# Kernel tuning notes

Measured on AMD Instinct MI355X. Metric: run time of the kernel, lower is better.

Reference implementation:

```python
import jax, jax.numpy as jnp
import numpy as np

N = 50000        # total nodes (random mix of disease type=1 and mirna type=0)
E = 1250000      # edges, avg degree 25
D_SIM = 256      # similarity feature dim (G.ndata['d_sim']/['m_sim'] width)
F_ATTN = 64      # feature_attn_size
SLOPE = 0.2      # leaky_relu negative slope


def setup_inputs() -> dict:
    key = jax.random.key(0)
    k = jax.random.split(key, 7)
    d_sim = jax.random.normal(k[0], (N, D_SIM), dtype=jnp.float32)
    m_sim = jax.random.normal(k[1], (N, D_SIM), dtype=jnp.float32)
    node_type = jax.random.randint(k[2], (N,), 0, 2, dtype=jnp.int32)
    src = jax.random.randint(k[3], (E,), 0, N)
    dst = jax.random.randint(k[4], (E,), 0, N)
    # xavier_normal with gain = calculate_gain('relu') = sqrt(2)
    scale = np.float32(np.sqrt(2.0) * np.sqrt(2.0 / (D_SIM + F_ATTN)))
    W_d = jax.random.normal(k[5], (D_SIM, F_ATTN), dtype=jnp.float32) * scale
    W_m = jax.random.normal(k[6], (D_SIM, F_ATTN), dtype=jnp.float32) * scale
    return {"d_sim": d_sim, "m_sim": m_sim, "W_d": W_d, "W_m": W_m,
            "node_type": node_type, "src": src, "dst": dst}


def reference(d_sim, m_sim, W_d, W_m, node_type, src, dst):
    # type-specific linear projection (dropout=0 -> identity)
    z_d = d_sim @ W_d                       # [N, F]
    z_m = m_sim @ W_m                       # [N, F]
    z = jnp.where((node_type == 1)[:, None], z_d, z_m)  # [N, F]

    # edge attention: leaky_relu(<z_src, z_dst>)
    z_src = z[src]                          # [E, F]
    e = jnp.sum(z_src * z[dst], axis=1)     # [E]
    e = jax.nn.leaky_relu(e, negative_slope=SLOPE)

    # segment softmax over incoming edges of each dst node
    e_max = jax.ops.segment_max(e, dst, num_segments=N)          # [N]
    e_max = jnp.where(jnp.isfinite(e_max), e_max, 0.0)           # empty segments
    ex = jnp.exp(e - e_max[dst])                                 # [E]
    denom = jax.ops.segment_sum(ex, dst, num_segments=N)         # [N]
    alpha = ex / jnp.maximum(denom[dst], 1e-16)                  # [E]

    # softmax-weighted neighbor aggregation, then ELU
    h = jax.ops.segment_sum(alpha[:, None] * z_src, dst, num_segments=N)  # [N, F]
    return jax.nn.elu(h)
```

## Files before the change

### kernel.cpp

```cpp
#include <hip/hip_runtime.h>
#include <math.h>


#define F 64
#define TM 128
#define TK 64
#define BSH 5
#define CHUNK 4096
#define CAP 1280
#define HCAP 1280

#define PROJ_LDS (128 * (TK + 1) * 4 + TK * F * 4)

__global__ void classify_kernel(const int* __restrict__ node_type, int* __restrict__ tcnt,
                                int* __restrict__ list0, int* __restrict__ list1, int n) {
    int i = blockIdx.x * 256 + threadIdx.x;
    if (i < n) {
        int lane = threadIdx.x & 63;
        int t = node_type[i];
        unsigned long long b1 = __ballot(t == 1);
        unsigned long long ba = __ballot(1);
        unsigned long long mlt = (1ull << lane) - 1ull;
        int r1 = __popcll(b1 & mlt);
        int r0 = __popcll(ba & ~b1 & mlt);
        int base0, base1;
        if (lane == 0) {
            base1 = atomicAdd(&tcnt[1], __popcll(b1));
            base0 = atomicAdd(&tcnt[0], __popcll(ba & ~b1));
        }
        base0 = __shfl(base0, 0, 64);
        base1 = __shfl(base1, 0, 64);
        if (t == 1) list1[base1 + r1] = i;
        else        list0[base0 + r0] = i;
    }
}

__global__ __launch_bounds__(256, 2)
void proj_scatter(const float* __restrict__ d_sim, const float* __restrict__ m_sim,
                  const float* __restrict__ W_d, const float* __restrict__ W_m,
                  const int* __restrict__ tcnt, const int* __restrict__ list0,
                  const int* __restrict__ list1, float* __restrict__ z,
                  const int* __restrict__ dst, const int* __restrict__ src,
                  int* __restrict__ bucket_count, int* __restrict__ bucket_data,
                  int e, int nbuk, int nsort) {
    __shared__ __align__(16) char smem[PROJ_LDS];
    int bid = blockIdx.x;

    if (bid < nsort) {
        int* hist  = (int*)smem;
        int* bbase = hist + 2048;
        int* rk    = bbase + 2048;
        for (int i = threadIdx.x; i < nbuk; i += 256) { hist[i] = 0; rk[i] = 0; }
        __syncthreads();
        int beg = bid * CHUNK, end = min(e, beg + CHUNK);
        for (int i = beg + (int)threadIdx.x * 4; i < end; i += 1024) {
            int4 d4 = *(const int4*)(dst + i);
            atomicAdd(&hist[d4.x >> BSH], 1);
            atomicAdd(&hist[d4.y >> BSH], 1);
            atomicAdd(&hist[d4.z >> BSH], 1);
            atomicAdd(&hist[d4.w >> BSH], 1);
        }
        __syncthreads();
        for (int i = threadIdx.x; i < nbuk; i += 256)
            bbase[i] = hist[i] ? atomicAdd(&bucket_count[i], hist[i]) : 0;
        __syncthreads();
        for (int i = beg + (int)threadIdx.x * 4; i < end; i += 1024) {
            int4 d4 = *(const int4*)(dst + i);
            int4 s4 = *(const int4*)(src + i);
            int b0 = d4.x >> BSH, b1 = d4.y >> BSH, b2 = d4.z >> BSH, b3 = d4.w >> BSH;
            int r0 = atomicAdd(&rk[b0], 1);
            int r1 = atomicAdd(&rk[b1], 1);
            int r2 = atomicAdd(&rk[b2], 1);
            int r3 = atomicAdd(&rk[b3], 1);
            int p0 = bbase[b0] + r0, p1 = bbase[b1] + r1;
            int p2 = bbase[b2] + r2, p3 = bbase[b3] + r3;
            if (p0 < CAP) bucket_data[(size_t)b0 * CAP + p0] = ((d4.x & 31) << 16) | s4.x;
            if (p1 < CAP) bucket_data[(size_t)b1 * CAP + p1] = ((d4.y & 31) << 16) | s4.y;
            if (p2 < CAP) bucket_data[(size_t)b2 * CAP + p2] = ((d4.z & 31) << 16) | s4.z;
            if (p3 < CAP) bucket_data[(size_t)b3 * CAP + p3] = ((d4.w & 31) << 16) | s4.w;
        }
        return;
    }

    int pb = bid - nsort;
    int ty = pb & 1;
    int cnt = tcnt[ty];
    int base = (pb >> 1) * TM;
    if (base >= cnt) return;
    const int*   list = ty ? list1 : list0;
    const float* A    = ty ? d_sim : m_sim;
    const float* W    = ty ? W_d   : W_m;

    float (*sA)[TK + 1] = (float (*)[TK + 1])smem;
    float (*sW)[F]      = (float (*)[F])(smem + 128 * (TK + 1) * 4);

    int rg = threadIdx.x >> 4;
    int cg = threadIdx.x & 15;

    int srow_node[8];
    #pragma unroll
    for (int j = 0; j < 8; j++) {
        int idx = (int)threadIdx.x + 256 * j;
        int li = base + (idx >> 4);
        if (li >= cnt) li = cnt - 1;
        srow_node[j] = list[li];
    }

    float acc[8][4] = {};
    for (int kc = 0; kc < 256; kc += TK) {
        __syncthreads();
        #pragma unroll
        for (int j = 0; j < 8; j++) {
            int idx = (int)threadIdx.x + 256 * j;
            int r = idx >> 4, f4 = idx & 15;
            float4 v = *(const float4*)(A + (size_t)srow_node[j] * 256 + kc + f4 * 4);
            sA[r][f4 * 4 + 0] = v.x;
            sA[r][f4 * 4 + 1] = v.y;
            sA[r][f4 * 4 + 2] = v.z;
            sA[r][f4 * 4 + 3] = v.w;
        }
        #pragma unroll
        for (int j = 0; j < 4; j++) {
            int idx = (int)threadIdx.x + 256 * j;
            int k = idx >> 4, f4 = idx & 15;
            float4 v = *(const float4*)(W + (size_t)(kc + k) * F + f4 * 4);
            *(float4*)&sW[k][f4 * 4] = v;
        }
        __syncthreads();
        #pragma unroll 4
        for (int k = 0; k < TK; k++) {
            float4 wv = *(const float4*)&sW[k][cg * 4];
            float a[8];
            #pragma unroll
            for (int i = 0; i < 8; i++) a[i] = sA[rg * 8 + i][k];
            #pragma unroll
            for (int i = 0; i < 8; i++) {
                acc[i][0] = fmaf(a[i], wv.x, acc[i][0]);
                acc[i][1] = fmaf(a[i], wv.y, acc[i][1]);
                acc[i][2] = fmaf(a[i], wv.z, acc[i][2]);
                acc[i][3] = fmaf(a[i], wv.w, acc[i][3]);
            }
        }
    }
    #pragma unroll
    for (int i = 0; i < 8; i++) {
        int li = base + rg * 8 + i;
        if (li < cnt) {
            int node = list[li];
            float4 v = {acc[i][0], acc[i][1], acc[i][2], acc[i][3]};
            *(float4*)(z + (size_t)node * F + cg * 4) = v;
        }
    }
}

__global__ __launch_bounds__(512)
void attn_fused(const float* __restrict__ z, const int* __restrict__ bucket_count,
                const int* __restrict__ bucket_data, float* __restrict__ out, int n) {
    __shared__ unsigned short ssrc[HCAP];
    __shared__ int cnt[32], excl[32], cur[32];
    int b = blockIdx.x;
    int dbase = b << BSH;
    const int* __restrict__ bd = bucket_data + (size_t)b * CAP;
    int len = min(bucket_count[b], CAP);
    int tid = threadIdx.x;

    if (tid < 32) { cnt[tid] = 0; cur[tid] = 0; }
    __syncthreads();
    for (int i = tid; i < len; i += 512)
        atomicAdd(&cnt[bd[i] >> 16], 1);
    __syncthreads();
    if (tid < 32) {
        int v = cnt[tid];
        int s = v;
        #pragma unroll
        for (int off = 1; off < 32; off <<= 1) {
            int t = __shfl_up(s, off, 32);
            if (tid >= off) s += t;
        }
        excl[tid] = s - v;
    }
    __syncthreads();
    for (int i = tid; i < len; i += 512) {
        int v = bd[i];
        int d5 = v >> 16;
        int r = atomicAdd(&cur[d5], 1);
        int pos = excl[d5] + r;
        if (pos < HCAP) ssrc[pos] = (unsigned short)(v & 0xFFFF);
    }
    __syncthreads();

    int lane = tid & 63;
    int wv = tid >> 6;
    int g = lane >> 4, r = lane & 15;
    for (int k = 0; k < 4; k++) {
        int d5 = wv + 8 * k;
        int node = dbase + d5;
        if (node >= n) continue;
        int lbeg = excl[d5];
        int lcnt = min(cnt[d5], max(0, HCAP - lbeg));
        float4 zd = ((const float4*)(z + (size_t)node * F))[r];
        float m = -3.402823466e38f, l = 0.f;
        float4 acc = {0.f, 0.f, 0.f, 0.f};
        for (int j = 0; j < lcnt; j += 4) {
            int jj = j + g;
            int s = ssrc[lbeg + min(jj, lcnt - 1)];
            float4 zc = ((const float4*)(z + (size_t)s * F))[r];
            float p = fmaf(zc.x, zd.x, fmaf(zc.y, zd.y, fmaf(zc.z, zd.z, zc.w * zd.w)));
            p += __shfl_xor(p, 1, 64);
            p += __shfl_xor(p, 2, 64);
            p += __shfl_xor(p, 4, 64);
            p += __shfl_xor(p, 8, 64);
            float e = (p > 0.f) ? p : 0.2f * p;
            if (jj >= lcnt) e = -INFINITY;
            float t = __expf(-fabsf(e - m));
            bool gt = (e > m);
            float sc = gt ? t : 1.f;
            float w  = gt ? 1.f : t;
            m = gt ? e : m;
            l = fmaf(l, sc, w);
            acc.x = fmaf(acc.x, sc, w * zc.x);
            acc.y = fmaf(acc.y, sc, w * zc.y);
            acc.z = fmaf(acc.z, sc, w * zc.z);
            acc.w = fmaf(acc.w, sc, w * zc.w);
        }
        #pragma unroll
        for (int off = 16; off <= 32; off <<= 1) {
            float om = __shfl_xor(m, off, 64);
            float ol = __shfl_xor(l, off, 64);
            float4 oa;
            oa.x = __shfl_xor(acc.x, off, 64);
            oa.y = __shfl_xor(acc.y, off, 64);
            oa.z = __shfl_xor(acc.z, off, 64);
            oa.w = __shfl_xor(acc.w, off, 64);
            float t = __expf(-fabsf(m - om));
            bool gt = (om > m);
            float sc = gt ? t : 1.f;
            float so = gt ? 1.f : t;
            m = gt ? om : m;
            l = fmaf(l, sc, ol * so);
            acc.x = fmaf(acc.x, sc, oa.x * so);
            acc.y = fmaf(acc.y, sc, oa.y * so);
            acc.z = fmaf(acc.z, sc, oa.z * so);
            acc.w = fmaf(acc.w, sc, oa.w * so);
        }
        float inv = 1.f / fmaxf(l, 1e-16f);
        float4 o;
        o.x = acc.x * inv; o.y = acc.y * inv; o.z = acc.z * inv; o.w = acc.w * inv;
        o.x = (o.x > 0.f) ? o.x : (__expf(o.x) - 1.f);
        o.y = (o.y > 0.f) ? o.y : (__expf(o.y) - 1.f);
        o.z = (o.z > 0.f) ? o.z : (__expf(o.z) - 1.f);
        o.w = (o.w > 0.f) ? o.w : (__expf(o.w) - 1.f);
        if (g == 0) ((float4*)(out + (size_t)node * F))[r] = o;
    }
}

extern "C" void kernel_launch(void* const* d_in, const int* in_sizes, int n_in,
                              void* d_out, int out_size, void* d_ws, size_t ws_size,
                              hipStream_t stream) {
    const float* d_sim     = (const float*)d_in[0];
    const float* m_sim     = (const float*)d_in[1];
    const float* W_d       = (const float*)d_in[2];
    const float* W_m       = (const float*)d_in[3];
    const int*   node_type = (const int*)d_in[4];
    const int*   src       = (const int*)d_in[5];
    const int*   dst       = (const int*)d_in[6];
    float* out = (float*)d_out;

    const int N = in_sizes[4];
    const int E = in_sizes[5];
    const int NBUK = (N + 31) >> BSH;

    char* ws = (char*)d_ws;
    int*   tcnt   = (int*)ws;
    int*   bcount = tcnt + 2;
    int    head   = (2 + 2048 + 3) & ~3;
    float* z      = (float*)(ws + (size_t)head * 4);
    int*   list0  = (int*)(z + (size_t)N * F);
    int*   list1  = list0 + N;
    int*   bdata  = list1 + N;

    hipMemsetAsync(tcnt, 0, (size_t)(2 + 2048) * sizeof(int), stream);

    dim3 blk(256);
    classify_kernel<<<dim3((N + 255) / 256), blk, 0, stream>>>(node_type, tcnt, list0, list1, N);

    int nsort = (E + CHUNK - 1) / CHUNK;
    int pgrid = 2 * ((N + TM - 1) / TM);
    proj_scatter<<<dim3(nsort + pgrid), blk, 0, stream>>>(d_sim, m_sim, W_d, W_m,
                                                          tcnt, list0, list1, z,
                                                          dst, src, bcount, bdata,
                                                          E, NBUK, nsort);
    attn_fused<<<dim3(NBUK), dim3(512), 0, stream>>>(z, bcount, bdata, out, N);
}
```

Before: 242.2 us.

## Fuse memset, classify, projection/scatter and attention into one cooperative persistent kernel

Replaces the memset plus three kernel launches with one cooperative persistent kernel that runs each phase in turn, separated by grid-wide syncs. Blocks are split between edge bucketing and the node projection inside a phase, and the attention phase loops over buckets with a grid-stride loop. The aim is to remove launch gaps and per-kernel ramp-up and tail. The cost is grid.sync overhead, a block size and occupancy bounded by the cooperative grid limit, and fewer blocks available for the heavy phases. If the cooperative launch is rejected, it falls back to the old multi-kernel path.

```diff
diff --git a/kernel.cpp b/kernel.cpp
--- a/kernel.cpp
+++ b/kernel.cpp
@@ -1,5 +1,8 @@
 #include <hip/hip_runtime.h>
+#include <hip/hip_cooperative_groups.h>
 #include <math.h>
+
+namespace cg = cooperative_groups;
 
 
 #define F 64
@@ -9,8 +12,267 @@
 #define CHUNK 4096
 #define CAP 1280
 #define HCAP 1280
+#define BLK 512
+#define SMEM_SZ 49664
 
 #define PROJ_LDS (128 * (TK + 1) * 4 + TK * F * 4)
+
+__global__ __launch_bounds__(BLK, 4)
+void mega(const float* __restrict__ d_sim, const float* __restrict__ m_sim,
+          const float* __restrict__ W_d, const float* __restrict__ W_m,
+          const int* __restrict__ node_type, const int* __restrict__ src,
+          const int* __restrict__ dst, float* __restrict__ out,
+          int* __restrict__ tcnt, int* __restrict__ bcount,
+          int* __restrict__ list0, int* __restrict__ list1,
+          float* __restrict__ z, int* __restrict__ bdata,
+          int n, int ne, int nbuk, int nchunk, int nscat) {
+    extern __shared__ __align__(16) char smem[];
+    cg::grid_group gg = cg::this_grid();
+    const int tid = threadIdx.x;
+    const int bid = blockIdx.x;
+    const int gsz = gridDim.x;
+
+    if (bid == 0) {
+        for (int i = tid; i < 2050; i += BLK) {
+            if (i < 2048) bcount[i] = 0;
+            else          tcnt[i - 2048] = 0;
+        }
+    }
+    __threadfence();
+    gg.sync();
+
+    for (int base = bid * BLK; base < n; base += gsz * BLK) {
+        int i = base + tid;
+        if (i < n) {
+            int lane = tid & 63;
+            int t = node_type[i];
+            unsigned long long b1 = __ballot(t == 1);
+            unsigned long long ba = __ballot(1);
+            unsigned long long mlt = (1ull << lane) - 1ull;
+            int r1 = __popcll(b1 & mlt);
+            int r0 = __popcll(ba & ~b1 & mlt);
+            int base0, base1;
+            if (lane == 0) {
+                base1 = atomicAdd(&tcnt[1], __popcll(b1));
+                base0 = atomicAdd(&tcnt[0], __popcll(ba & ~b1));
+            }
+            base0 = __shfl(base0, 0, 64);
+            base1 = __shfl(base1, 0, 64);
+            if (t == 1) list1[base1 + r1] = i;
+            else        list0[base0 + r0] = i;
+        }
+    }
+    __threadfence();
+    gg.sync();
+
+    if (bid < nscat) {
+        int* hist  = (int*)smem;
+        int* bbase = hist + 2048;
+        int* rk    = bbase + 2048;
+        for (int c = bid; c < nchunk; c += nscat) {
+            for (int i = tid; i < nbuk; i += BLK) { hist[i] = 0; rk[i] = 0; }
+            __syncthreads();
+            int beg = c * CHUNK, end = min(ne, beg + CHUNK);
+            for (int i = beg + tid * 4; i < end; i += BLK * 4) {
+                int4 d4 = *(const int4*)(dst + i);
+                atomicAdd(&hist[d4.x >> BSH], 1);
+                atomicAdd(&hist[d4.y >> BSH], 1);
+                atomicAdd(&hist[d4.z >> BSH], 1);
+                atomicAdd(&hist[d4.w >> BSH], 1);
+            }
+            __syncthreads();
+            for (int i = tid; i < nbuk; i += BLK)
+                bbase[i] = hist[i] ? atomicAdd(&bcount[i], hist[i]) : 0;
+            __syncthreads();
+            for (int i = beg + tid * 4; i < end; i += BLK * 4) {
+                int4 d4 = *(const int4*)(dst + i);
+                int4 s4 = *(const int4*)(src + i);
+                int b0 = d4.x >> BSH, b1 = d4.y >> BSH, b2 = d4.z >> BSH, b3 = d4.w >> BSH;
+                int r0 = atomicAdd(&rk[b0], 1);
+                int r1 = atomicAdd(&rk[b1], 1);
+                int r2 = atomicAdd(&rk[b2], 1);
+                int r3 = atomicAdd(&rk[b3], 1);
+                int p0 = bbase[b0] + r0, p1 = bbase[b1] + r1;
+                int p2 = bbase[b2] + r2, p3 = bbase[b3] + r3;
+                if (p0 < CAP) bdata[(size_t)b0 * CAP + p0] = ((d4.x & 31) << 16) | s4.x;
+                if (p1 < CAP) bdata[(size_t)b1 * CAP + p1] = ((d4.y & 31) << 16) | s4.y;
+                if (p2 < CAP) bdata[(size_t)b2 * CAP + p2] = ((d4.z & 31) << 16) | s4.z;
+                if (p3 < CAP) bdata[(size_t)b3 * CAP + p3] = ((d4.w & 31) << 16) | s4.w;
+            }
+            __syncthreads();
+        }
+    } else {
+        float (*sA)[TK + 1] = (float (*)[TK + 1])smem;
+        float (*sW)[F]      = (float (*)[F])(smem + 128 * (TK + 1) * 4);
+        int rg = tid >> 4, cg4 = tid & 15;
+        int ntasks = 2 * ((n + TM - 1) / TM);
+        int pblk = gsz - nscat;
+        for (int t = bid - nscat; t < ntasks; t += pblk) {
+            int ty = t & 1;
+            int cnt = tcnt[ty];
+            int base = (t >> 1) * TM;
+            if (base >= cnt) continue;
+            const int*   list = ty ? list1 : list0;
+            const float* A    = ty ? d_sim : m_sim;
+            const float* W    = ty ? W_d   : W_m;
+            int snode[4];
+            #pragma unroll
+            for (int j = 0; j < 4; j++) {
+                int li = base + ((tid + BLK * j) >> 4);
+                if (li >= cnt) li = cnt - 1;
+                snode[j] = list[li];
+            }
+            float acc[4][4] = {};
+            for (int kc = 0; kc < 256; kc += TK) {
+                __syncthreads();
+                #pragma unroll
+                for (int j = 0; j < 4; j++) {
+                    int idx = tid + BLK * j;
+                    int r = idx >> 4, f4 = idx & 15;
+                    float4 v = *(const float4*)(A + (size_t)snode[j] * 256 + kc + f4 * 4);
+                    sA[r][f4 * 4 + 0] = v.x;
+                    sA[r][f4 * 4 + 1] = v.y;
+                    sA[r][f4 * 4 + 2] = v.z;
+                    sA[r][f4 * 4 + 3] = v.w;
+                }
+                #pragma unroll
+                for (int j = 0; j < 2; j++) {
+                    int idx = tid + BLK * j;
+                    int k = idx >> 4, f4 = idx & 15;
+                    *(float4*)&sW[k][f4 * 4] =
+                        *(const float4*)(W + (size_t)(kc + k) * F + f4 * 4);
+                }
+                __syncthreads();
+                #pragma unroll 4
+                for (int k = 0; k < TK; k++) {
+                    float4 wv = *(const float4*)&sW[k][cg4 * 4];
+                    float a[4];
+                    #pragma unroll
+                    for (int i = 0; i < 4; i++) a[i] = sA[rg * 4 + i][k];
+                    #pragma unroll
+                    for (int i = 0; i < 4; i++) {
+                        acc[i][0] = fmaf(a[i], wv.x, acc[i][0]);
+                        acc[i][1] = fmaf(a[i], wv.y, acc[i][1]);
+                        acc[i][2] = fmaf(a[i], wv.z, acc[i][2]);
+                        acc[i][3] = fmaf(a[i], wv.w, acc[i][3]);
+                    }
+                }
+            }
+            __syncthreads();
+            #pragma unroll
+            for (int i = 0; i < 4; i++) {
+                int li = base + rg * 4 + i;
+                if (li < cnt) {
+                    int node = list[li];
+                    float4 v = {acc[i][0], acc[i][1], acc[i][2], acc[i][3]};
+                    *(float4*)(z + (size_t)node * F + cg4 * 4) = v;
+                }
+            }
+        }
+    }
+    __threadfence();
+    gg.sync();
+
+    {
+        unsigned short* ssrc = (unsigned short*)smem;
+        int* cnt  = (int*)(smem + 2560);
+        int* excl = cnt + 32;
+        int* cur  = excl + 32;
+        int lane = tid & 63;
+        int wv = tid >> 6;
+        int g = lane >> 4, r = lane & 15;
+        for (int b = bid; b < nbuk; b += gsz) {
+            __syncthreads();
+            int dbase = b << BSH;
+            const int* __restrict__ bd = bdata + (size_t)b * CAP;
+            int len = min(bcount[b], CAP);
+            if (tid < 32) { cnt[tid] = 0; cur[tid] = 0; }
+            __syncthreads();
+            for (int i = tid; i < len; i += BLK)
+                atomicAdd(&cnt[bd[i] >> 16], 1);
+            __syncthreads();
+            if (tid < 32) {
+                int v = cnt[tid];
+                int s = v;
+                #pragma unroll
+                for (int off = 1; off < 32; off <<= 1) {
+                    int t = __shfl_up(s, off, 32);
+                    if (tid >= off) s += t;
+                }
+                excl[tid] = s - v;
+            }
+            __syncthreads();
+            for (int i = tid; i < len; i += BLK) {
+                int v = bd[i];
+                int d5 = v >> 16;
+                int rr = atomicAdd(&cur[d5], 1);
+                int pos = excl[d5] + rr;
+                if (pos < HCAP) ssrc[pos] = (unsigned short)(v & 0xFFFF);
+            }
+            __syncthreads();
+            for (int k = 0; k < 4; k++) {
+                int d5 = wv + 8 * k;
+                int node = dbase + d5;
+                if (node >= n) continue;
+                int lbeg = excl[d5];
+                int lcnt = min(cnt[d5], max(0, HCAP - lbeg));
+                float4 zd = ((const float4*)(z + (size_t)node * F))[r];
+                float m = -3.402823466e38f, l = 0.f;
+                float4 acc = {0.f, 0.f, 0.f, 0.f};
+                for (int j = 0; j < lcnt; j += 4) {
+                    int jj = j + g;
+                    int s = ssrc[lbeg + min(jj, lcnt - 1)];
+                    float4 zc = ((const float4*)(z + (size_t)s * F))[r];
+                    float p = fmaf(zc.x, zd.x, fmaf(zc.y, zd.y, fmaf(zc.z, zd.z, zc.w * zd.w)));
+                    p += __shfl_xor(p, 1, 64);
+                    p += __shfl_xor(p, 2, 64);
+                    p += __shfl_xor(p, 4, 64);
+                    p += __shfl_xor(p, 8, 64);
+                    float e = (p > 0.f) ? p : 0.2f * p;
+                    if (jj >= lcnt) e = -INFINITY;
+                    float t = __expf(-fabsf(e - m));
+                    bool gt = (e > m);
+                    float sc = gt ? t : 1.f;
+                    float w  = gt ? 1.f : t;
+                    m = gt ? e : m;
+                    l = fmaf(l, sc, w);
+                    acc.x = fmaf(acc.x, sc, w * zc.x);
+                    acc.y = fmaf(acc.y, sc, w * zc.y);
+                    acc.z = fmaf(acc.z, sc, w * zc.z);
+                    acc.w = fmaf(acc.w, sc, w * zc.w);
+                }
+                #pragma unroll
+                for (int off = 16; off <= 32; off <<= 1) {
+                    float om = __shfl_xor(m, off, 64);
+                    float ol = __shfl_xor(l, off, 64);
+                    float4 oa;
+                    oa.x = __shfl_xor(acc.x, off, 64);
+                    oa.y = __shfl_xor(acc.y, off, 64);
+                    oa.z = __shfl_xor(acc.z, off, 64);
+                    oa.w = __shfl_xor(acc.w, off, 64);
+                    float t = __expf(-fabsf(m - om));
+                    bool gt = (om > m);
+                    float sc = gt ? t : 1.f;
+                    float so = gt ? 1.f : t;
+                    m = gt ? om : m;
+                    l = fmaf(l, sc, ol * so);
+                    acc.x = fmaf(acc.x, sc, oa.x * so);
+                    acc.y = fmaf(acc.y, sc, oa.y * so);
+                    acc.z = fmaf(acc.z, sc, oa.z * so);
+                    acc.w = fmaf(acc.w, sc, oa.w * so);
+                }
+                float inv = 1.f / fmaxf(l, 1e-16f);
+                float4 o;
+                o.x = acc.x * inv; o.y = acc.y * inv; o.z = acc.z * inv; o.w = acc.w * inv;
+                o.x = (o.x > 0.f) ? o.x : (__expf(o.x) - 1.f);
+                o.y = (o.y > 0.f) ? o.y : (__expf(o.y) - 1.f);
+                o.z = (o.z > 0.f) ? o.z : (__expf(o.z) - 1.f);
+                o.w = (o.w > 0.f) ? o.w : (__expf(o.w) - 1.f);
+                if (g == 0) ((float4*)(out + (size_t)node * F))[r] = o;
+            }
+        }
+    }
+}
 
 __global__ void classify_kernel(const int* __restrict__ node_type, int* __restrict__ tcnt,
                                 int* __restrict__ list0, int* __restrict__ list1, int n) {
@@ -266,9 +528,10 @@
     const int*   dst       = (const int*)d_in[6];
     float* out = (float*)d_out;
 
-    const int N = in_sizes[4];
-    const int E = in_sizes[5];
-    const int NBUK = (N + 31) >> BSH;
+    int N = in_sizes[4];
+    int E = in_sizes[5];
+    int NBUK = (N + 31) >> BSH;
+    int NCHUNK = (E + CHUNK - 1) / CHUNK;
 
     char* ws = (char*)d_ws;
     int*   tcnt   = (int*)ws;
@@ -279,11 +542,48 @@
     int*   list1  = list0 + N;
     int*   bdata  = list1 + N;
 
+    static int coop_grid = 0;
+    if (coop_grid == 0) {
+        int dev = 0;
+        (void)hipGetDevice(&dev);
+        int coop = 0, ncu = 0, nb = 0;
+        (void)hipDeviceGetAttribute(&coop, hipDeviceAttributeCooperativeLaunch, dev);
+        (void)hipDeviceGetAttribute(&ncu, hipDeviceAttributeMultiprocessorCount, dev);
+        hipError_t oe = hipOccupancyMaxActiveBlocksPerMultiprocessor(
+            &nb, (const void*)mega, BLK, (size_t)SMEM_SZ);
+        if (coop && ncu > 0 && oe == hipSuccess && nb > 0) {
+            long g = (long)nb * ncu;
+            coop_grid = (int)(g > 2048 ? 2048 : g);
+        } else {
+            coop_grid = -1;
+        }
+    }
+
+    if (coop_grid > 0) {
+        int gsz = coop_grid;
+        int nscat = gsz / 3; if (nscat < 1) nscat = 1; if (nscat >= gsz) nscat = gsz - 1;
+        void* args[] = {&d_sim, &m_sim, &W_d, &W_m, &node_type, &src, &dst, &out,
+                        &tcnt, &bcount, &list0, &list1, &z, &bdata,
+                        &N, &E, &NBUK, &NCHUNK, &nscat};
+        hipError_t e = hipLaunchCooperativeKernel((const void*)mega, dim3(gsz), dim3(BLK),
+                                                  args, SMEM_SZ, stream);
+        if (e == hipSuccess) return;
+        int gsz2 = gsz > 256 ? 256 : gsz / 2;
+        if (gsz2 >= 8) {
+            int nscat2 = gsz2 / 3; if (nscat2 < 1) nscat2 = 1;
+            void* args2[] = {&d_sim, &m_sim, &W_d, &W_m, &node_type, &src, &dst, &out,
+                             &tcnt, &bcount, &list0, &list1, &z, &bdata,
+                             &N, &E, &NBUK, &NCHUNK, &nscat2};
+            e = hipLaunchCooperativeKernel((const void*)mega, dim3(gsz2), dim3(BLK),
+                                           args2, SMEM_SZ, stream);
+            if (e == hipSuccess) { coop_grid = gsz2; return; }
+        }
+        coop_grid = -1;
+    }
+
     hipMemsetAsync(tcnt, 0, (size_t)(2 + 2048) * sizeof(int), stream);
-
     dim3 blk(256);
     classify_kernel<<<dim3((N + 255) / 256), blk, 0, stream>>>(node_type, tcnt, list0, list1, N);
-
     int nsort = (E + CHUNK - 1) / CHUNK;
     int pgrid = 2 * ((N + TM - 1) / TM);
     proj_scatter<<<dim3(nsort + pgrid), blk, 0, stream>>>(d_sim, m_sim, W_d, W_m,
```

After: 541.0 us. 2.23x slower.
